# Performance work log

Hardware: AMD Instinct MI355X
Metric: run time of the kernel (lower is better)

The kernel has to match this reference:

```python
import jax, jax.numpy as jnp
import numpy as np
from jax import lax

K = 16
SIGMA2 = 1.0  # sigma=1.0 squared
EPS = 1e-06


def setup_inputs() -> dict:
    key = jax.random.key(0)
    xyz = jax.random.normal(key, (4, 3, 4096), dtype=jnp.float32)
    return {"xyz": xyz}


def reference(xyz):
    # xyz: (B, 3, N)
    B, _, N = xyz.shape
    pts = jnp.transpose(xyz, (0, 2, 1))  # (B, N, 3)

    sq = jnp.sum(pts * pts, axis=-1)  # (B, N)
    d2 = sq[:, :, None] + sq[:, None, :] - 2.0 * jnp.einsum("bnd,bmd->bnm", pts, pts)

    # k nearest neighbors (smallest distance, includes self like torch knn on same set)
    _, idx = lax.top_k(-d2, K)  # idx: (B, N, K)

    # gather neighbor coordinates and recompute exact squared distance (faithful to source)
    neighbors = jax.vmap(lambda p, i: p[i])(pts, idx)  # (B, N, K, 3)
    diff = pts[:, :, None, :] - neighbors
    dist2 = jnp.sum(diff * diff, axis=-1)  # (B, N, K)
    weights = jnp.exp(-dist2 / (2.0 * SIGMA2))

    # scatter k-sparse weights into dense adjacency (topk indices per row are unique)
    bb = jnp.arange(B)[:, None, None]
    ii = jnp.arange(N)[None, :, None]
    A = jnp.zeros((B, N, N), dtype=xyz.dtype).at[bb, ii, idx].set(weights)
    A = 0.5 * (A + jnp.swapaxes(A, 1, 2))

    # symmetric normalized Laplacian L = I - D^{-1/2} A D^{-1/2} (diag scaling via broadcast)
    D = jnp.clip(jnp.sum(A, axis=-1), EPS, None)
    d_is = D ** -0.5  # (B, N)
    L = jnp.eye(N, dtype=xyz.dtype)[None] - d_is[:, :, None] * A * d_is[:, None, :]
    return L
```

## Files before the change

### kernel.cpp

```cpp
#include <hip/hip_runtime.h>
#include <math.h>

#pragma clang fp contract(off)

#define NPTS 4096
#define KNN  16
#define RPBK 32
#define KT   1024
#define CAP  128
#define CAPIN 64
#define SPILLCAP 262144
#define RROWS 4

__device__ __forceinline__ unsigned okey(float f) {
    f = f + 0.0f;
    unsigned u = __float_as_uint(f);
    return u ^ (((unsigned)((int)u >> 31)) | 0x80000000u);
}

__device__ __forceinline__ unsigned long long wmin64(unsigned long long v) {
    for (int o = 32; o > 0; o >>= 1) { unsigned long long w = __shfl_xor(v, o); v = w < v ? w : v; }
    return v;
}

__device__ __forceinline__ float disv(const float* __restrict__ Dsum, int i) {
    return 1.0f / sqrtf(fmaxf(Dsum[i], 1e-6f));
}

__global__ void zero_kernel(float* __restrict__ p, int n) {
    int i = blockIdx.x * blockDim.x + threadIdx.x;
    if (i < n) p[i] = 0.0f;
}

__device__ __forceinline__ float thresh16(float k, int lane) {
    int rank = 0;
    for (int s = 0; s < 64; ++s) {
        float ks = __shfl(k, s);
        rank += (ks < k || (ks == k && s < lane)) ? 1 : 0;
    }
    unsigned long long m = __ballot(rank == 15);
    return __shfl(k, __ffsll(m) - 1);
}

__device__ __forceinline__ int select16(const float4* __restrict__ spts,
                                        const int* __restrict__ list,
                                        int cnt2, float4 P, int lane) {
    if (cnt2 <= 64) {
        float key = __builtin_huge_valf();
        int m = -1;
        if (lane < cnt2) {
            m = list[lane];
            float4 Q = spts[m];
            float dot = (P.x * Q.x + P.y * Q.y) + P.z * Q.z;
            key = (P.w + Q.w) - 2.0f * dot;
        }
        int rank = 0;
        for (int s = 0; s < 64; ++s) {
            float ks = __shfl(key, s);
            rank += (ks < key || (ks == key && s < lane)) ? 1 : 0;
        }
        return __builtin_amdgcn_ds_permute(rank << 2, m);
    }
    if (cnt2 <= CAP) {
        unsigned long long e0 = ~0ull, e1 = ~0ull;
        if (lane < cnt2) {
            int m = list[lane]; float4 Q = spts[m];
            float dot = (P.x * Q.x + P.y * Q.y) + P.z * Q.z;
            float d2  = (P.w + Q.w) - 2.0f * dot;
            e0 = ((unsigned long long)okey(d2) << 32) | (unsigned)m;
        }
        if (lane + 64 < cnt2) {
            int m = list[lane + 64]; float4 Q = spts[m];
            float dot = (P.x * Q.x + P.y * Q.y) + P.z * Q.z;
            float d2  = (P.w + Q.w) - 2.0f * dot;
            e1 = ((unsigned long long)okey(d2) << 32) | (unsigned)m;
        }
        int selm = -1;
        unsigned long long c = e0 < e1 ? e0 : e1;
        for (int r = 0; r < KNN; ++r) {
            unsigned long long mn = wmin64(c);
            if (c == mn) {
                if (e0 == mn) e0 = ~0ull; else e1 = ~0ull;
                c = e0 < e1 ? e0 : e1;
            }
            if (lane == r) selm = (int)(unsigned)(mn & 0xFFFFFFFFull);
        }
        return selm;
    }
    unsigned long long last = 0; int selm = -1;
    for (int r = 0; r < KNN; ++r) {
        unsigned long long bestp = ~0ull;
        for (int i = 0; i < NPTS / 64; ++i) {
            int m = i * 64 + lane;
            float4 Q  = spts[m];
            float dot = (P.x * Q.x + P.y * Q.y) + P.z * Q.z;
            float d2  = (P.w + Q.w) - 2.0f * dot;
            unsigned long long key = ((unsigned long long)okey(d2) << 32) | (unsigned)m;
            if (key > last && key < bestp) bestp = key;
        }
        unsigned long long mn = wmin64(bestp);
        if (lane == r) selm = (int)(unsigned)(mn & 0xFFFFFFFFull);
        last = mn;
    }
    return selm;
}

__device__ __forceinline__ void emit_row(int rowg, int b, int selm, float4 P,
                                         const float4* __restrict__ spts,
                                         float* __restrict__ Dsum,
                                         int* __restrict__ idx_out,
                                         float* __restrict__ w_out,
                                         int* __restrict__ cnt,
                                         int* __restrict__ inc,
                                         int* __restrict__ spillc,
                                         int* __restrict__ spill,
                                         int do_inc, int lane) {
    float wgt = 0.0f;
    if (lane < KNN) {
        int j = selm;
        float4 Q = spts[j];
        float dx = P.x - Q.x, dy = P.y - Q.y, dz = P.z - Q.z;
        float dist2 = (dx * dx + dy * dy) + dz * dz;
        wgt = expf(-(dist2 * 0.5f));
        size_t base = (size_t)rowg * KNN + lane;
        idx_out[base] = j;
        w_out[base]   = wgt;
        int jg = (b << 12) + j;
        atomicAdd(&Dsum[jg], 0.5f * wgt);
        if (do_inc) {
            int pos = atomicAdd(&cnt[jg], 1);
            if (pos < CAPIN) {
                inc[(size_t)jg * CAPIN + pos] = (int)base;
            } else {
                int sp = atomicAdd(spillc, 1);
                if (sp < SPILLCAP) spill[sp] = (int)base;
            }
        }
    }
    float rs = wgt;
    for (int o = 32; o > 0; o >>= 1) rs += __shfl_xor(rs, o);
    if (lane == 0) atomicAdd(&Dsum[rowg], 0.5f * rs);
}

__global__ __launch_bounds__(KT, 4) void knn_kernel(const float* __restrict__ xyz,
                                                    float* __restrict__ Dsum,
                                                    int* __restrict__ idx_out,
                                                    float* __restrict__ w_out,
                                                    int* __restrict__ cnt,
                                                    int* __restrict__ inc,
                                                    int* __restrict__ spillc,
                                                    int* __restrict__ spill,
                                                    int do_inc) {
    __shared__ float4 spts[NPTS];
    __shared__ int    lists[RPBK][CAP];

    const int t    = threadIdx.x;
    const int lane = t & 63;
    const int wv   = t >> 6;
    const int row0 = blockIdx.x * RPBK + 2 * wv;
    const int b    = row0 >> 12;
    const float* X = xyz + (size_t)b * 3 * NPTS;

    for (int i = t; i < NPTS; i += KT) {
        float x = X[i], y = X[NPTS + i], z = X[2 * NPTS + i];
        spts[i] = make_float4(x, y, z, (x * x + y * y) + z * z);
    }
    __syncthreads();

    const float4 PA = spts[row0 & (NPTS - 1)];
    const float4 PB = spts[(row0 + 1) & (NPTS - 1)];

    float bA = __builtin_huge_valf(), bB = __builtin_huge_valf();
    for (int i = 0; i < NPTS / 64; ++i) {
        float4 Q  = spts[i * 64 + lane];
        float dotA = (PA.x * Q.x + PA.y * Q.y) + PA.z * Q.z;
        float d2A  = (PA.w + Q.w) - 2.0f * dotA;
        float dotB = (PB.x * Q.x + PB.y * Q.y) + PB.z * Q.z;
        float d2B  = (PB.w + Q.w) - 2.0f * dotB;
        bA = fminf(bA, d2A);
        bB = fminf(bB, d2B);
    }
    const float TA = thresh16(bA, lane);
    const float TB = thresh16(bB, lane);

    int* listA = &lists[2 * wv][0];
    int* listB = &lists[2 * wv + 1][0];
    int cA = 0, cB = 0;
    for (int i = 0; i < NPTS / 64; ++i) {
        int m = i * 64 + lane;
        float4 Q  = spts[m];
        float dotA = (PA.x * Q.x + PA.y * Q.y) + PA.z * Q.z;
        float d2A  = (PA.w + Q.w) - 2.0f * dotA;
        float dotB = (PB.x * Q.x + PB.y * Q.y) + PB.z * Q.z;
        float d2B  = (PB.w + Q.w) - 2.0f * dotB;
        bool pA = d2A <= TA;
        unsigned long long balA = __ballot(pA);
        if (pA) {
            int pos = cA + __popcll(balA & ((1ull << lane) - 1ull));
            if (pos < CAP) listA[pos] = m;
        }
        cA += (int)__popcll(balA);
        bool pB = d2B <= TB;
        unsigned long long balB = __ballot(pB);
        if (pB) {
            int pos = cB + __popcll(balB & ((1ull << lane) - 1ull));
            if (pos < CAP) listB[pos] = m;
        }
        cB += (int)__popcll(balB);
    }

    int selA = select16(spts, listA, cA, PA, lane);
    int selB = select16(spts, listB, cB, PB, lane);
    emit_row(row0,     b, selA, PA, spts, Dsum, idx_out, w_out,
             cnt, inc, spillc, spill, do_inc, lane);
    emit_row(row0 + 1, b, selB, PB, spts, Dsum, idx_out, w_out,
             cnt, inc, spillc, spill, do_inc, lane);
}

__global__ __launch_bounds__(1024, 4) void row_kernel(const int* __restrict__ idxb,
                                                      const float* __restrict__ wb,
                                                      const float* __restrict__ Dsum,
                                                      const int* __restrict__ cnt,
                                                      const int* __restrict__ inc,
                                                      const int* __restrict__ spillc,
                                                      const int* __restrict__ spill,
                                                      float* __restrict__ L) {
    __shared__ float row[RROWS * NPTS];
    const int r0 = blockIdx.x * RROWS;
    const int b  = r0 >> 12;

    float4* row4 = (float4*)row;
    for (int i = threadIdx.x; i < RROWS * NPTS / 4; i += 1024)
        row4[i] = make_float4(0.0f, 0.0f, 0.0f, 0.0f);
    __syncthreads();

    const int rr = threadIdx.x >> 8;
    const int tt = threadIdx.x & 255;
    const int r  = r0 + rr;
    float* myrow = row + rr * NPTS;
    const float dn = disv(Dsum, r);

    if (tt < KNN) {
        int g = r * KNN + tt;
        int j = idxb[g];
        float v = -0.5f * wb[g] * dn * disv(Dsum, (b << 12) + j);
        atomicAdd(&myrow[j], v);
    }
    int c = cnt[r];
    if (c > CAPIN) c = CAPIN;
    for (int i = tt; i < c; i += 256) {
        int g   = inc[(size_t)r * CAPIN + i];
        int src = g >> 4;
        float v = -0.5f * wb[g] * disv(Dsum, src) * dn;
        atomicAdd(&myrow[src & (NPTS - 1)], v);
    }

    int sc = spillc[0];
    if (sc > 0) {
        if (sc > SPILLCAP) sc = SPILLCAP;
        for (int i = threadIdx.x; i < sc; i += 1024) {
            int g   = spill[i];
            int src = g >> 4;
            int jg  = ((src >> 12) << 12) + idxb[g];
            if (jg >= r0 && jg < r0 + RROWS) {
                float v = -0.5f * wb[g] * disv(Dsum, src) * disv(Dsum, jg);
                atomicAdd(&row[(jg - r0) * NPTS + (src & (NPTS - 1))], v);
            }
        }
    }
    __syncthreads();

    const int n0 = r0 & (NPTS - 1);
    float4* Lr = (float4*)(L + (size_t)b * NPTS * NPTS + (size_t)n0 * NPTS);
    for (int q = threadIdx.x; q < RROWS * NPTS / 4; q += 1024) {
        float4 v = row4[q];
        int n = n0 + (q >> 10);
        if ((q & 1023) == (n >> 2)) ((float*)&v)[n & 3] += 1.0f;
        Lr[q] = v;
    }
}

__global__ void dis_kernel(const float* __restrict__ Dsum, float* __restrict__ dis, int n) {
    int i = blockIdx.x * blockDim.x + threadIdx.x;
    if (i < n) dis[i] = 1.0f / sqrtf(fmaxf(Dsum[i], 1e-6f));
}

__global__ __launch_bounds__(256) void fill_kernel(float4* __restrict__ L4, size_t T4) {
    size_t g4     = (size_t)blockIdx.x * blockDim.x + threadIdx.x;
    size_t stride = (size_t)gridDim.x * blockDim.x;
    for (; g4 < T4; g4 += stride) {
        size_t g = g4 << 2;
        int o    = (int)(g & (size_t)(NPTS * (size_t)NPTS - 1));
        int row  = o >> 12;
        int col0 = o & (NPTS - 1);
        float4 v;
        v.x = (row == col0    ) ? 1.0f : 0.0f;
        v.y = (row == col0 + 1) ? 1.0f : 0.0f;
        v.z = (row == col0 + 2) ? 1.0f : 0.0f;
        v.w = (row == col0 + 3) ? 1.0f : 0.0f;
        L4[g4] = v;
    }
}

__global__ __launch_bounds__(256) void scatter_kernel(const int* __restrict__ idxb,
                                                      const float* __restrict__ wb,
                                                      const float* __restrict__ dis,
                                                      float* __restrict__ L) {
    int g   = blockIdx.x * 256 + threadIdx.x;
    int row = g >> 4;
    int b   = row >> 12;
    int n   = row & (NPTS - 1);
    int j   = idxb[g];
    float v = -0.5f * wb[g] * dis[row] * dis[(b << 12) + j];
    float* Lb = L + (size_t)b * NPTS * NPTS;
    atomicAdd(Lb + (size_t)n * NPTS + j, v);
    atomicAdd(Lb + (size_t)j * NPTS + n, v);
}

extern "C" void kernel_launch(void* const* d_in, const int* in_sizes, int n_in,
                              void* d_out, int out_size, void* d_ws, size_t ws_size,
                              hipStream_t stream) {
    const float* xyz = (const float*)d_in[0];
    const int B  = in_sizes[0] / (3 * NPTS);
    const int BN = B * NPTS;

    float* Dsum   = (float*)d_ws;
    int*   cnt    = (int*)(Dsum + BN);
    int*   spillc = cnt + BN;
    int*   idxb   = (int*)(spillc + 16);
    float* wb     = (float*)(idxb + (size_t)BN * KNN);
    int*   inc    = (int*)(wb + (size_t)BN * KNN);
    int*   spill  = inc + (size_t)BN * CAPIN;
    float* L      = (float*)d_out;

    size_t need = ((size_t)BN * (2 + 2 * KNN + CAPIN) + 16 + SPILLCAP) * 4;
    const int fused = (ws_size >= need);

    if (fused) {
        int nz = 2 * BN + 16;
        zero_kernel<<<(nz + 255) / 256, 256, 0, stream>>>(Dsum, nz);
        knn_kernel<<<BN / RPBK, KT, 0, stream>>>(xyz, Dsum, idxb, wb,
                                                 cnt, inc, spillc, spill, 1);
        row_kernel<<<BN / RROWS, 1024, 0, stream>>>(idxb, wb, Dsum,
                                                    cnt, inc, spillc, spill, L);
    } else {
        float* fDsum = (float*)d_ws;
        float* fdis  = fDsum + BN;
        int*   fidx  = (int*)(fdis + BN);
        float* fwb   = (float*)(fidx + (size_t)BN * KNN);
        zero_kernel<<<BN / 256, 256, 0, stream>>>(fDsum, BN);
        knn_kernel<<<BN / RPBK, KT, 0, stream>>>(xyz, fDsum, fidx, fwb,
                                                 nullptr, nullptr, nullptr, nullptr, 0);
        dis_kernel<<<BN / 256, 256, 0, stream>>>(fDsum, fdis, BN);
        size_t T4 = (size_t)B * NPTS * NPTS / 4;
        fill_kernel<<<8192, 256, 0, stream>>>((float4*)d_out, T4);
        scatter_kernel<<<(BN * KNN) / 256, 256, 0, stream>>>(fidx, fwb, fdis, L);
    }
}
```

Before: 358.2 us.

## Split shared point cloud into SoA arrays, raise occupancy, use nontemporal L stores

Shared point storage moves from float4 (with a precomputed norm) to three separate x/y/z float arrays, and the squared norm is recomputed on the fly. This cuts LDS use from 64KB to 48KB so the launch bound can ask for 8 blocks per CU instead of 4. The rank loops are unrolled, and the dense Laplacian row write now uses nontemporal stores to avoid polluting cache. In exchange each scan iteration does three scalar LDS loads plus extra FLOPs for the norm instead of one vector load, and the higher occupancy target may force register spills.

```diff
diff --git a/kernel.cpp b/kernel.cpp
--- a/kernel.cpp
+++ b/kernel.cpp
@@ -12,6 +12,8 @@
 #define SPILLCAP 262144
 #define RROWS 4
 
+typedef float nfloat4 __attribute__((ext_vector_type(4)));
+
 __device__ __forceinline__ unsigned okey(float f) {
     f = f + 0.0f;
     unsigned u = __float_as_uint(f);
@@ -34,6 +36,7 @@
 
 __device__ __forceinline__ float thresh16(float k, int lane) {
     int rank = 0;
+#pragma unroll
     for (int s = 0; s < 64; ++s) {
         float ks = __shfl(k, s);
         rank += (ks < k || (ks == k && s < lane)) ? 1 : 0;
@@ -42,7 +45,9 @@
     return __shfl(k, __ffsll(m) - 1);
 }
 
-__device__ __forceinline__ int select16(const float4* __restrict__ spts,
+__device__ __forceinline__ int select16(const float* __restrict__ sx,
+                                        const float* __restrict__ sy,
+                                        const float* __restrict__ sz,
                                         const int* __restrict__ list,
                                         int cnt2, float4 P, int lane) {
     if (cnt2 <= 64) {
@@ -50,11 +55,13 @@
         int m = -1;
         if (lane < cnt2) {
             m = list[lane];
-            float4 Q = spts[m];
-            float dot = (P.x * Q.x + P.y * Q.y) + P.z * Q.z;
-            key = (P.w + Q.w) - 2.0f * dot;
+            float qx = sx[m], qy = sy[m], qz = sz[m];
+            float qw = (qx * qx + qy * qy) + qz * qz;
+            float dot = (P.x * qx + P.y * qy) + P.z * qz;
+            key = (P.w + qw) - 2.0f * dot;
         }
         int rank = 0;
+#pragma unroll
         for (int s = 0; s < 64; ++s) {
             float ks = __shfl(key, s);
             rank += (ks < key || (ks == key && s < lane)) ? 1 : 0;
@@ -64,15 +71,19 @@
     if (cnt2 <= CAP) {
         unsigned long long e0 = ~0ull, e1 = ~0ull;
         if (lane < cnt2) {
-            int m = list[lane]; float4 Q = spts[m];
-            float dot = (P.x * Q.x + P.y * Q.y) + P.z * Q.z;
-            float d2  = (P.w + Q.w) - 2.0f * dot;
+            int m = list[lane];
+            float qx = sx[m], qy = sy[m], qz = sz[m];
+            float qw = (qx * qx + qy * qy) + qz * qz;
+            float dot = (P.x * qx + P.y * qy) + P.z * qz;
+            float d2  = (P.w + qw) - 2.0f * dot;
             e0 = ((unsigned long long)okey(d2) << 32) | (unsigned)m;
         }
         if (lane + 64 < cnt2) {
-            int m = list[lane + 64]; float4 Q = spts[m];
-            float dot = (P.x * Q.x + P.y * Q.y) + P.z * Q.z;
-            float d2  = (P.w + Q.w) - 2.0f * dot;
+            int m = list[lane + 64];
+            float qx = sx[m], qy = sy[m], qz = sz[m];
+            float qw = (qx * qx + qy * qy) + qz * qz;
+            float dot = (P.x * qx + P.y * qy) + P.z * qz;
+            float d2  = (P.w + qw) - 2.0f * dot;
             e1 = ((unsigned long long)okey(d2) << 32) | (unsigned)m;
         }
         int selm = -1;
@@ -92,9 +103,10 @@
         unsigned long long bestp = ~0ull;
         for (int i = 0; i < NPTS / 64; ++i) {
             int m = i * 64 + lane;
-            float4 Q  = spts[m];
-            float dot = (P.x * Q.x + P.y * Q.y) + P.z * Q.z;
-            float d2  = (P.w + Q.w) - 2.0f * dot;
+            float qx = sx[m], qy = sy[m], qz = sz[m];
+            float qw = (qx * qx + qy * qy) + qz * qz;
+            float dot = (P.x * qx + P.y * qy) + P.z * qz;
+            float d2  = (P.w + qw) - 2.0f * dot;
             unsigned long long key = ((unsigned long long)okey(d2) << 32) | (unsigned)m;
             if (key > last && key < bestp) bestp = key;
         }
@@ -106,7 +118,9 @@
 }
 
 __device__ __forceinline__ void emit_row(int rowg, int b, int selm, float4 P,
-                                         const float4* __restrict__ spts,
+                                         const float* __restrict__ sx,
+                                         const float* __restrict__ sy,
+                                         const float* __restrict__ sz,
                                          float* __restrict__ Dsum,
                                          int* __restrict__ idx_out,
                                          float* __restrict__ w_out,
@@ -118,8 +132,7 @@
     float wgt = 0.0f;
     if (lane < KNN) {
         int j = selm;
-        float4 Q = spts[j];
-        float dx = P.x - Q.x, dy = P.y - Q.y, dz = P.z - Q.z;
+        float dx = P.x - sx[j], dy = P.y - sy[j], dz = P.z - sz[j];
         float dist2 = (dx * dx + dy * dy) + dz * dz;
         wgt = expf(-(dist2 * 0.5f));
         size_t base = (size_t)rowg * KNN + lane;
@@ -142,7 +155,7 @@
     if (lane == 0) atomicAdd(&Dsum[rowg], 0.5f * rs);
 }
 
-__global__ __launch_bounds__(KT, 4) void knn_kernel(const float* __restrict__ xyz,
+__global__ __launch_bounds__(KT, 8) void knn_kernel(const float* __restrict__ xyz,
                                                     float* __restrict__ Dsum,
                                                     int* __restrict__ idx_out,
                                                     float* __restrict__ w_out,
@@ -151,8 +164,8 @@
                                                     int* __restrict__ spillc,
                                                     int* __restrict__ spill,
                                                     int do_inc) {
-    __shared__ float4 spts[NPTS];
-    __shared__ int    lists[RPBK][CAP];
+    __shared__ float sx[NPTS], sy[NPTS], sz[NPTS];
+    __shared__ int   lists[RPBK][CAP];
 
     const int t    = threadIdx.x;
     const int lane = t & 63;
@@ -162,21 +175,26 @@
     const float* X = xyz + (size_t)b * 3 * NPTS;
 
     for (int i = t; i < NPTS; i += KT) {
-        float x = X[i], y = X[NPTS + i], z = X[2 * NPTS + i];
-        spts[i] = make_float4(x, y, z, (x * x + y * y) + z * z);
+        sx[i] = X[i]; sy[i] = X[NPTS + i]; sz[i] = X[2 * NPTS + i];
     }
     __syncthreads();
 
-    const float4 PA = spts[row0 & (NPTS - 1)];
-    const float4 PB = spts[(row0 + 1) & (NPTS - 1)];
+    const int ra = row0 & (NPTS - 1), rb = (row0 + 1) & (NPTS - 1);
+    float4 PA, PB;
+    PA.x = sx[ra]; PA.y = sy[ra]; PA.z = sz[ra];
+    PA.w = (PA.x * PA.x + PA.y * PA.y) + PA.z * PA.z;
+    PB.x = sx[rb]; PB.y = sy[rb]; PB.z = sz[rb];
+    PB.w = (PB.x * PB.x + PB.y * PB.y) + PB.z * PB.z;
 
     float bA = __builtin_huge_valf(), bB = __builtin_huge_valf();
     for (int i = 0; i < NPTS / 64; ++i) {
-        float4 Q  = spts[i * 64 + lane];
-        float dotA = (PA.x * Q.x + PA.y * Q.y) + PA.z * Q.z;
-        float d2A  = (PA.w + Q.w) - 2.0f * dotA;
-        float dotB = (PB.x * Q.x + PB.y * Q.y) + PB.z * Q.z;
-        float d2B  = (PB.w + Q.w) - 2.0f * dotB;
+        int m = i * 64 + lane;
+        float qx = sx[m], qy = sy[m], qz = sz[m];
+        float qw = (qx * qx + qy * qy) + qz * qz;
+        float dotA = (PA.x * qx + PA.y * qy) + PA.z * qz;
+        float d2A  = (PA.w + qw) - 2.0f * dotA;
+        float dotB = (PB.x * qx + PB.y * qy) + PB.z * qz;
+        float d2B  = (PB.w + qw) - 2.0f * dotB;
         bA = fminf(bA, d2A);
         bB = fminf(bB, d2B);
     }
@@ -188,11 +206,12 @@
     int cA = 0, cB = 0;
     for (int i = 0; i < NPTS / 64; ++i) {
         int m = i * 64 + lane;
-        float4 Q  = spts[m];
-        float dotA = (PA.x * Q.x + PA.y * Q.y) + PA.z * Q.z;
-        float d2A  = (PA.w + Q.w) - 2.0f * dotA;
-        float dotB = (PB.x * Q.x + PB.y * Q.y) + PB.z * Q.z;
-        float d2B  = (PB.w + Q.w) - 2.0f * dotB;
+        float qx = sx[m], qy = sy[m], qz = sz[m];
+        float qw = (qx * qx + qy * qy) + qz * qz;
+        float dotA = (PA.x * qx + PA.y * qy) + PA.z * qz;
+        float d2A  = (PA.w + qw) - 2.0f * dotA;
+        float dotB = (PB.x * qx + PB.y * qy) + PB.z * qz;
+        float d2B  = (PB.w + qw) - 2.0f * dotB;
         bool pA = d2A <= TA;
         unsigned long long balA = __ballot(pA);
         if (pA) {
@@ -209,11 +228,11 @@
         cB += (int)__popcll(balB);
     }
 
-    int selA = select16(spts, listA, cA, PA, lane);
-    int selB = select16(spts, listB, cB, PB, lane);
-    emit_row(row0,     b, selA, PA, spts, Dsum, idx_out, w_out,
+    int selA = select16(sx, sy, sz, listA, cA, PA, lane);
+    int selB = select16(sx, sy, sz, listB, cB, PB, lane);
+    emit_row(row0,     b, selA, PA, sx, sy, sz, Dsum, idx_out, w_out,
              cnt, inc, spillc, spill, do_inc, lane);
-    emit_row(row0 + 1, b, selB, PB, spts, Dsum, idx_out, w_out,
+    emit_row(row0 + 1, b, selB, PB, sx, sy, sz, Dsum, idx_out, w_out,
              cnt, inc, spillc, spill, do_inc, lane);
 }
 
@@ -271,12 +290,13 @@
     __syncthreads();
 
     const int n0 = r0 & (NPTS - 1);
-    float4* Lr = (float4*)(L + (size_t)b * NPTS * NPTS + (size_t)n0 * NPTS);
+    nfloat4* Lr = (nfloat4*)(L + (size_t)b * NPTS * NPTS + (size_t)n0 * NPTS);
+    const nfloat4* row4n = (const nfloat4*)row;
     for (int q = threadIdx.x; q < RROWS * NPTS / 4; q += 1024) {
-        float4 v = row4[q];
+        nfloat4 v = row4n[q];
         int n = n0 + (q >> 10);
-        if ((q & 1023) == (n >> 2)) ((float*)&v)[n & 3] += 1.0f;
-        Lr[q] = v;
+        if ((q & 1023) == (n >> 2)) v[n & 3] += 1.0f;
+        __builtin_nontemporal_store(v, &Lr[q]);
     }
 }
 
```

Measured after the change: 363.3 us. No clear change (+1.4%).
